# Performance work log

Hardware: AMD Instinct MI355X
Metric: run time of the kernel (lower is better)

## Reference

```python
import jax, jax.numpy as jnp
import numpy as np

PENETRATION_W = 10.0
STABILITY_W = 1.0
ENERGY_W = 0.1
MIN_DIST = 0.05

B, T, N, D = 16, 100, 128, 3

def setup_inputs() -> dict:
    key = jax.random.key(0)
    k1, k2, k3 = jax.random.split(key, 3)
    trajectories = jax.random.normal(k1, (B, T, N, D), dtype=jnp.float32)
    velocities = jax.random.normal(k2, (B, T, N, D), dtype=jnp.float32)
    forces = jax.random.normal(k3, (B, T, N, D), dtype=jnp.float32)
    return {"trajectories": trajectories, "velocities": velocities, "forces": forces}

def _penetration_loss(trajectories):
    b, t, n, _ = trajectories.shape
    pos = trajectories[..., :3]                                   # [B,T,N,3]
    diff = pos[:, :, :, None, :] - pos[:, :, None, :, :]          # [B,T,N,N,3]
    d2 = jnp.sum(diff * diff, axis=-1)                            # [B,T,N,N]
    mask = jnp.triu(jnp.ones((n, n), dtype=bool), k=1)            # strictly i<j
    # avoid sqrt(0) on diagonal for safe gradients; masked out below
    dist = jnp.sqrt(jnp.where(mask, d2, 1.0))
    pen = jax.nn.relu(MIN_DIST - dist) * mask                     # [B,T,N,N]
    # original: sum over (t, i<j) of mean over batch
    total = jnp.mean(jnp.sum(pen, axis=(1, 2, 3)))
    return total / (t * n * (n - 1) / 2)

def _stability_loss(velocities):
    return jnp.mean(jnp.linalg.norm(velocities[:, -5:], axis=-1))

def _energy_loss(positions, velocities, forces):
    kinetic_start = 0.5 * jnp.mean(jnp.sum(velocities[:, 0] ** 2, axis=-1))
    kinetic_end = 0.5 * jnp.mean(jnp.sum(velocities[:, -1] ** 2, axis=-1))
    displacements = positions[:, 1:] - positions[:, :-1]
    work = jnp.mean(jnp.sum(forces[:, :-1] * displacements, axis=-1))
    return jnp.abs(kinetic_end - kinetic_start - work)

def reference(trajectories, velocities, forces):
    loss = PENETRATION_W * _penetration_loss(trajectories)
    loss = loss + STABILITY_W * _stability_loss(velocities)
    loss = loss + ENERGY_W * _energy_loss(trajectories, velocities, forces)
    return loss
```

## Files before the change

kernel.cpp:

```cpp
#include <hip/hip_runtime.h>
#include <math.h>

constexpr int B = 16, T = 100, N = 128;
constexpr float MIN_DIST  = 0.05f;
constexpr float MIN_DIST2 = MIN_DIST * MIN_DIST;

constexpr int THREADS = 256;
constexpr int G       = 800;

constexpr int PER_B = T * N * 3;
constexpr int PER_T = N * 3;

constexpr int WORK_V4_PER_B = (T - 1) * N * 3 / 4;
constexpr int WORK_V4 = B * WORK_V4_PER_B;
constexpr int KE_V4_PER_SLICE = N * 3 / 4;
constexpr int KE_V4  = 2 * B * KE_V4_PER_SLICE;
constexpr int STAB_V = B * 5 * N;
constexpr int MISC_TOTAL = WORK_V4 + STAB_V + KE_V4;

constexpr int WORK_N = B * (T - 1) * N;

__device__ __forceinline__ float wave_sum(float v) {
#pragma unroll
    for (int off = 32; off > 0; off >>= 1) v += __shfl_down(v, off, 64);
    return v;
}

__global__ __launch_bounds__(THREADS, 4) void physics_one(
    const float* __restrict__ traj, const float* __restrict__ vel,
    const float* __restrict__ frc, float* __restrict__ ws)
{
    __shared__ float  sraw[2 * PER_T];
    __shared__ float4 spos[2][N];
    __shared__ float  red[5][4];

    const int tid  = threadIdx.x;
    const int bid  = blockIdx.x;
    const int lane = tid & 63;
    const int wv   = tid >> 6;

    const int v = bid * THREADS + tid;
    int cat = 3, which = 0;
    float4 mf, mt0, mt1;
    float  e0 = 0.f, e1 = 0.f, e2 = 0.f;
    {
        const float4* t4 = (const float4*)traj;
        const float4* f4 = (const float4*)frc;
        const float4* v4 = (const float4*)vel;
        if (v < WORK_V4) {
            cat = 0;
            const int b = v / WORK_V4_PER_B;
            const int r = v - b * WORK_V4_PER_B;
            const int base = b * (PER_B / 4) + r;
            mf  = f4[base];
            mt0 = t4[base];
            mt1 = t4[base + PER_T / 4];
        } else if (v < WORK_V4 + STAB_V) {
            cat = 1;
            const int s2 = v - WORK_V4;
            const int b  = s2 / 640;
            const int r  = s2 - b * 640;
            const int e  = b * PER_B + 95 * PER_T + r * 3;
            e0 = vel[e]; e1 = vel[e + 1]; e2 = vel[e + 2];
        } else if (v < MISC_TOTAL) {
            cat = 2;
            const int s2 = v - WORK_V4 - STAB_V;
            which        = s2 / 1536;
            const int rr = s2 - which * 1536;
            const int b  = rr / KE_V4_PER_SLICE;
            const int r  = rr - b * KE_V4_PER_SLICE;
            mf = v4[b * (PER_B / 4) + which * (99 * PER_T / 4) + r];
        }
    }

    if (tid < 192) {
        const int s  = tid >= 96;
        const int r  = tid - s * 96;
        const int pb = bid + s * G;
        ((float4*)sraw)[tid] = ((const float4*)traj)[pb * (PER_T / 4) + r];
    }
    __syncthreads();
    {
        const int s = tid >> 7, p = tid & (N - 1);
        const float* rb = sraw + s * PER_T;
        spos[s][p] = make_float4(rb[p * 3], rb[p * 3 + 1], rb[p * 3 + 2], 0.f);
    }
    __syncthreads();

    const int i    = tid & (N - 1);
    const int half = tid >> 7;
    const int k0   = 1 + half * 32;
    const int k1   = 32 + half * 31;
    float pen = 0.f;
#pragma unroll
    for (int s = 0; s < 2; ++s) {
        const float4 pi = spos[s][i];
#pragma unroll 8
        for (int k = k0; k <= k1; ++k) {
            const int j = (i + k) & (N - 1);
            const float4 pj = spos[s][j];
            const float dx = pi.x - pj.x, dy = pi.y - pj.y, dz = pi.z - pj.z;
            const float d2 = dx * dx + dy * dy + dz * dz;
            const bool h = d2 < MIN_DIST2;
            if (__builtin_expect(__any(h), 0))
                if (h) pen += MIN_DIST - sqrtf(d2);
        }
        if (half) {
            const float4 pj = spos[s][(i + 64) & (N - 1)];
            const float dx = pi.x - pj.x, dy = pi.y - pj.y, dz = pi.z - pj.z;
            const float d2 = dx * dx + dy * dy + dz * dz;
            const bool h = (d2 < MIN_DIST2) & (i < 64);
            if (__builtin_expect(__any(h), 0))
                if (h) pen += MIN_DIST - sqrtf(d2);
        }
    }

    float sw = 0.f, ss = 0.f, ka = 0.f, kb = 0.f;
    if (cat == 0) {
        sw = mf.x * (mt1.x - mt0.x) + mf.y * (mt1.y - mt0.y)
           + mf.z * (mt1.z - mt0.z) + mf.w * (mt1.w - mt0.w);
    } else if (cat == 1) {
        ss = sqrtf(e0 * e0 + e1 * e1 + e2 * e2);
    } else if (cat == 2) {
        const float k = mf.x * mf.x + mf.y * mf.y + mf.z * mf.z + mf.w * mf.w;
        if (which) kb = k; else ka = k;
    }

    float vals[5] = {pen, sw, ss, ka, kb};
#pragma unroll
    for (int q = 0; q < 5; ++q) {
        const float w = wave_sum(vals[q]);
        if (lane == 0) red[q][wv] = w;
    }
    __syncthreads();
    if (tid < 5)
        ws[tid * G + bid] = red[tid][0] + red[tid][1] + red[tid][2] + red[tid][3];
}

__global__ __launch_bounds__(THREADS) void physics_fin(
    const float* __restrict__ ws, float* __restrict__ out)
{
    __shared__ float red[5][4];
    const int tid = threadIdx.x, lane = tid & 63, wv = tid >> 6;
    float acc[5] = {0.f, 0.f, 0.f, 0.f, 0.f};
    for (int idx = tid; idx < G; idx += THREADS) {
#pragma unroll
        for (int q = 0; q < 5; ++q) acc[q] += ws[q * G + idx];
    }
#pragma unroll
    for (int q = 0; q < 5; ++q) {
        const float w = wave_sum(acc[q]);
        if (lane == 0) red[q][wv] = w;
    }
    __syncthreads();
    if (tid == 0) {
        const float pen_t = red[0][0] + red[0][1] + red[0][2] + red[0][3];
        const float wk    = red[1][0] + red[1][1] + red[1][2] + red[1][3];
        const float st    = red[2][0] + red[2][1] + red[2][2] + red[2][3];
        const float k0s   = red[3][0] + red[3][1] + red[3][2] + red[3][3];
        const float k1s   = red[4][0] + red[4][1] + red[4][2] + red[4][3];
        const float pen_loss  = pen_t / (float)((long long)B * T * (N * (N - 1) / 2));
        const float stab_loss = st / (float)STAB_V;
        const float ke_s = 0.5f * k0s / (float)(B * N);
        const float ke_e = 0.5f * k1s / (float)(B * N);
        const float work = wk / (float)WORK_N;
        out[0] = 10.0f * pen_loss + stab_loss + 0.1f * fabsf(ke_e - ke_s - work);
    }
}

extern "C" void kernel_launch(void* const* d_in, const int* in_sizes, int n_in,
                              void* d_out, int out_size, void* d_ws, size_t ws_size,
                              hipStream_t stream) {
    const float* traj = (const float*)d_in[0];
    const float* vel  = (const float*)d_in[1];
    const float* frc  = (const float*)d_in[2];
    float* out = (float*)d_out;
    float* ws  = (float*)d_ws;

    physics_one<<<G, THREADS, 0, stream>>>(traj, vel, frc, ws);
    physics_fin<<<1, THREADS, 0, stream>>>(ws, out);
}
```

Baseline: 72.09 us.

## Launch one block per timestep and confine misc reductions to leading blocks

Changes the main kernel from 800 blocks handling two timesteps each to 1600 blocks handling one timestep each for the pairwise penetration check. The work, stability and kinetic terms are now computed only in the first blocks that exactly tile that work, and those blocks write to a separate workspace region. The finish kernel reduces the two regions separately. The aim is more parallelism and less serial work per block, at the cost of more blocks and more partial sums to reduce.

```diff
diff --git a/kernel.cpp b/kernel.cpp
--- a/kernel.cpp
+++ b/kernel.cpp
@@ -5,9 +5,8 @@
 constexpr float MIN_DIST  = 0.05f;
 constexpr float MIN_DIST2 = MIN_DIST * MIN_DIST;
 
-constexpr int THREADS = 256;
-constexpr int G       = 800;
-
+constexpr int THREADS    = 256;
+constexpr int PEN_BLOCKS = B * T;
 constexpr int PER_B = T * N * 3;
 constexpr int PER_T = N * 3;
 
@@ -16,9 +15,13 @@
 constexpr int KE_V4_PER_SLICE = N * 3 / 4;
 constexpr int KE_V4  = 2 * B * KE_V4_PER_SLICE;
 constexpr int STAB_V = B * 5 * N;
-constexpr int MISC_TOTAL = WORK_V4 + STAB_V + KE_V4;
+constexpr int MISC_TOTAL  = WORK_V4 + STAB_V + KE_V4;
+constexpr int MISC_BLOCKS = MISC_TOTAL / THREADS;
+static_assert(MISC_BLOCKS * THREADS == MISC_TOTAL, "misc must tile exactly");
 
 constexpr int WORK_N = B * (T - 1) * N;
+
+constexpr int MISC_OFF = PEN_BLOCKS;
 
 __device__ __forceinline__ float wave_sum(float v) {
 #pragma unroll
@@ -26,24 +29,25 @@
     return v;
 }
 
-__global__ __launch_bounds__(THREADS, 4) void physics_one(
+__global__ __launch_bounds__(THREADS) void physics_one(
     const float* __restrict__ traj, const float* __restrict__ vel,
     const float* __restrict__ frc, float* __restrict__ ws)
 {
-    __shared__ float  sraw[2 * PER_T];
-    __shared__ float4 spos[2][N];
+    __shared__ float  sraw[PER_T];
+    __shared__ float4 spos[N];
     __shared__ float  red[5][4];
 
     const int tid  = threadIdx.x;
     const int bid  = blockIdx.x;
     const int lane = tid & 63;
     const int wv   = tid >> 6;
+    const bool has_misc = (bid < MISC_BLOCKS);
 
-    const int v = bid * THREADS + tid;
     int cat = 3, which = 0;
     float4 mf, mt0, mt1;
     float  e0 = 0.f, e1 = 0.f, e2 = 0.f;
-    {
+    if (has_misc) {
+        const int v = bid * THREADS + tid;
         const float4* t4 = (const float4*)traj;
         const float4* f4 = (const float4*)frc;
         const float4* v4 = (const float4*)vel;
@@ -62,7 +66,7 @@
             const int r  = s2 - b * 640;
             const int e  = b * PER_B + 95 * PER_T + r * 3;
             e0 = vel[e]; e1 = vel[e + 1]; e2 = vel[e + 2];
-        } else if (v < MISC_TOTAL) {
+        } else {
             cat = 2;
             const int s2 = v - WORK_V4 - STAB_V;
             which        = s2 / 1536;
@@ -73,46 +77,36 @@
         }
     }
 
-    if (tid < 192) {
-        const int s  = tid >= 96;
-        const int r  = tid - s * 96;
-        const int pb = bid + s * G;
-        ((float4*)sraw)[tid] = ((const float4*)traj)[pb * (PER_T / 4) + r];
-    }
+    if (tid < PER_T / 4)
+        ((float4*)sraw)[tid] = ((const float4*)traj)[bid * (PER_T / 4) + tid];
     __syncthreads();
-    {
-        const int s = tid >> 7, p = tid & (N - 1);
-        const float* rb = sraw + s * PER_T;
-        spos[s][p] = make_float4(rb[p * 3], rb[p * 3 + 1], rb[p * 3 + 2], 0.f);
-    }
+    if (tid < N)
+        spos[tid] = make_float4(sraw[tid * 3], sraw[tid * 3 + 1], sraw[tid * 3 + 2], 0.f);
     __syncthreads();
 
     const int i    = tid & (N - 1);
     const int half = tid >> 7;
     const int k0   = 1 + half * 32;
     const int k1   = 32 + half * 31;
+    const float4 pi = spos[i];
     float pen = 0.f;
-#pragma unroll
-    for (int s = 0; s < 2; ++s) {
-        const float4 pi = spos[s][i];
 #pragma unroll 8
-        for (int k = k0; k <= k1; ++k) {
-            const int j = (i + k) & (N - 1);
-            const float4 pj = spos[s][j];
-            const float dx = pi.x - pj.x, dy = pi.y - pj.y, dz = pi.z - pj.z;
-            const float d2 = dx * dx + dy * dy + dz * dz;
-            const bool h = d2 < MIN_DIST2;
-            if (__builtin_expect(__any(h), 0))
-                if (h) pen += MIN_DIST - sqrtf(d2);
-        }
-        if (half) {
-            const float4 pj = spos[s][(i + 64) & (N - 1)];
-            const float dx = pi.x - pj.x, dy = pi.y - pj.y, dz = pi.z - pj.z;
-            const float d2 = dx * dx + dy * dy + dz * dz;
-            const bool h = (d2 < MIN_DIST2) & (i < 64);
-            if (__builtin_expect(__any(h), 0))
-                if (h) pen += MIN_DIST - sqrtf(d2);
-        }
+    for (int k = k0; k <= k1; ++k) {
+        const int j = (i + k) & (N - 1);
+        const float4 pj = spos[j];
+        const float dx = pi.x - pj.x, dy = pi.y - pj.y, dz = pi.z - pj.z;
+        const float d2 = dx * dx + dy * dy + dz * dz;
+        const bool h = d2 < MIN_DIST2;
+        if (__builtin_expect(__any(h), 0))
+            if (h) pen += MIN_DIST - sqrtf(d2);
+    }
+    if (half) {
+        const float4 pj = spos[(i + 64) & (N - 1)];
+        const float dx = pi.x - pj.x, dy = pi.y - pj.y, dz = pi.z - pj.z;
+        const float d2 = dx * dx + dy * dy + dz * dz;
+        const bool h = (d2 < MIN_DIST2) & (i < 64);
+        if (__builtin_expect(__any(h), 0))
+            if (h) pen += MIN_DIST - sqrtf(d2);
     }
 
     float sw = 0.f, ss = 0.f, ka = 0.f, kb = 0.f;
@@ -126,15 +120,24 @@
         if (which) kb = k; else ka = k;
     }
 
-    float vals[5] = {pen, sw, ss, ka, kb};
+    {
+        const float w = wave_sum(pen);
+        if (lane == 0) red[0][wv] = w;
+    }
+    if (has_misc) {
+        float vals[4] = {sw, ss, ka, kb};
 #pragma unroll
-    for (int q = 0; q < 5; ++q) {
-        const float w = wave_sum(vals[q]);
-        if (lane == 0) red[q][wv] = w;
+        for (int q = 0; q < 4; ++q) {
+            const float w = wave_sum(vals[q]);
+            if (lane == 0) red[q + 1][wv] = w;
+        }
     }
     __syncthreads();
-    if (tid < 5)
-        ws[tid * G + bid] = red[tid][0] + red[tid][1] + red[tid][2] + red[tid][3];
+    if (tid == 0)
+        ws[bid] = red[0][0] + red[0][1] + red[0][2] + red[0][3];
+    if (has_misc && tid < 4)
+        ws[MISC_OFF + tid * MISC_BLOCKS + bid] =
+            red[tid + 1][0] + red[tid + 1][1] + red[tid + 1][2] + red[tid + 1][3];
 }
 
 __global__ __launch_bounds__(THREADS) void physics_fin(
@@ -142,15 +145,23 @@
 {
     __shared__ float red[5][4];
     const int tid = threadIdx.x, lane = tid & 63, wv = tid >> 6;
-    float acc[5] = {0.f, 0.f, 0.f, 0.f, 0.f};
-    for (int idx = tid; idx < G; idx += THREADS) {
+
+    float p = 0.f;
+    for (int idx = tid; idx < PEN_BLOCKS; idx += THREADS) p += ws[idx];
+    float m[4] = {0.f, 0.f, 0.f, 0.f};
+    for (int idx = tid; idx < MISC_BLOCKS; idx += THREADS) {
 #pragma unroll
-        for (int q = 0; q < 5; ++q) acc[q] += ws[q * G + idx];
+        for (int q = 0; q < 4; ++q) m[q] += ws[MISC_OFF + q * MISC_BLOCKS + idx];
+    }
+
+    {
+        const float w = wave_sum(p);
+        if (lane == 0) red[0][wv] = w;
     }
 #pragma unroll
-    for (int q = 0; q < 5; ++q) {
-        const float w = wave_sum(acc[q]);
-        if (lane == 0) red[q][wv] = w;
+    for (int q = 0; q < 4; ++q) {
+        const float w = wave_sum(m[q]);
+        if (lane == 0) red[q + 1][wv] = w;
     }
     __syncthreads();
     if (tid == 0) {
@@ -177,6 +188,6 @@
     float* out = (float*)d_out;
     float* ws  = (float*)d_ws;
 
-    physics_one<<<G, THREADS, 0, stream>>>(traj, vel, frc, ws);
+    physics_one<<<PEN_BLOCKS, THREADS, 0, stream>>>(traj, vel, frc, ws);
     physics_fin<<<1, THREADS, 0, stream>>>(ws, out);
 }
```

New measurement: 69.83 us. 1.03x faster.
